# Performance work log

Hardware: AMD Instinct MI355X
Metric: run time of the kernel (lower is better)

Reference implementation:

```python
import jax, jax.numpy as jnp
import numpy as np

B, N, E = 16, 2048, 256


def setup_inputs() -> dict:
    key = jax.random.key(0)
    ks = jax.random.split(key, 9)
    locs = jax.random.uniform(ks[0], (B, N, 2), dtype=jnp.float32)
    probe = jax.random.randint(ks[1], (B, N), 0, 2).astype(bool)
    probe = probe.at[:, 0].set(True)  # guarantee >=1 probe per instance
    s = 0.02
    W_node = jax.random.normal(ks[2], (2, E), dtype=jnp.float32) * s
    b_node = jax.random.normal(ks[3], (E,), dtype=jnp.float32) * s
    W_dist = jax.random.normal(ks[4], (1, E), dtype=jnp.float32) * s
    b_dist = jax.random.normal(ks[5], (E,), dtype=jnp.float32) * s
    W_out = jax.random.normal(ks[6], (2 * E, E), dtype=jnp.float32) * s
    b_out = jax.random.normal(ks[7], (E,), dtype=jnp.float32) * s
    return {
        "locs": locs, "probe": probe,
        "W_node": W_node, "b_node": b_node,
        "W_dist": W_dist, "b_dist": b_dist,
        "W_out": W_out, "b_out": b_out,
    }


def _cdist(x):
    # pairwise euclidean distance [B,N,N] with safe sqrt (0-grad at 0)
    sq = jnp.sum(x * x, axis=-1)                       # [B,N]
    d2 = sq[:, :, None] + sq[:, None, :] - 2.0 * jnp.einsum("bnd,bmd->bnm", x, x)
    d2 = jnp.maximum(d2, 0.0)
    pos = d2 > 0.0
    return jnp.where(pos, jnp.sqrt(jnp.where(pos, d2, 1.0)), 0.0)


def reference(locs, probe, W_node, b_node, W_dist, b_dist, W_out, b_out):
    node_emb = locs @ W_node + b_node                  # [B,N,E]
    dist = _cdist(locs)                                # [B,N,N]
    # rows i that are NOT probes are set to +inf, then min over rows (dim=1)
    dist = jnp.where(probe[:, :, None], dist, jnp.inf)
    min_dist = jnp.min(dist, axis=1)                   # [B,N] dist to nearest probe
    dist_emb = min_dist[..., None] @ W_dist + b_dist   # [B,N,E]
    cat = jnp.concatenate([node_emb, dist_emb], axis=-1)
    return cat @ W_out + b_out                         # [B,N,E]
```

## Files before the change

kernel.cpp:

```cpp
#include <hip/hip_runtime.h>
#include <hip/hip_bf16.h>

#define BSZ  16
#define NPTS 2048
#define EDIM 256
#define QB   64
#define FPB  16

__global__ __launch_bounds__(256) void fold_part(
    const float* __restrict__ Wn,
    const float* __restrict__ bn,
    const float* __restrict__ Wd,
    const float* __restrict__ bd,
    const float* __restrict__ Wo,
    float* __restrict__ ws)
{
    const int e   = threadIdx.x;
    const int blk = blockIdx.x;
    float a = 0.f, b = 0.f, c = 0.f, d = 0.f;
#pragma unroll
    for (int kk = 0; kk < EDIM / FPB; ++kk) {
        const int k = blk * (EDIM / FPB) + kk;
        const float wt = Wo[k * EDIM + e];
        const float wb = Wo[(EDIM + k) * EDIM + e];
        a = fmaf(Wn[k],        wt, a);
        b = fmaf(Wn[EDIM + k], wt, b);
        d = fmaf(bn[k],        wt, d);
        c = fmaf(Wd[k],        wb, c);
        d = fmaf(bd[k],        wb, d);
    }
    float* o = ws + blk * 4 * EDIM;
    o[0 * EDIM + e] = a;
    o[1 * EDIM + e] = b;
    o[2 * EDIM + e] = c;
    o[3 * EDIM + e] = d;
}

__global__ __launch_bounds__(256) void mdpp_main(
    const float* __restrict__ locs,
    const int*   __restrict__ probe,
    const float* __restrict__ ws,
    const float* __restrict__ bo,
    float*       __restrict__ out)
{
    __shared__ __align__(16) float2 plist[NPTS + 2];
    __shared__ float  folded_lds[4 * EDIM];
    __shared__ int    pcount;
    __shared__ float  partmin[4][QB];
    __shared__ float  xq[QB], yq[QB], dq[QB];

    const int t   = threadIdx.x;
    const int bid = blockIdx.x;
    const int b   = bid >> 5;
    const int n0  = (bid & 31) * QB;

    if (t == 0) pcount = 0;
    __syncthreads();

    const float2* lb = reinterpret_cast<const float2*>(locs) + (size_t)b * NPTS;

#pragma unroll
    for (int jj = 0; jj < NPTS / 256; ++jj) {
        const int j = jj * 256 + t;
        if (probe[b * NPTS + j] != 0) {
            const int idx = atomicAdd(&pcount, 1);
            plist[idx] = lb[j];
        }
    }
    if (t < QB) {
        const float2 p = lb[n0 + t];
        xq[t] = p.x;
        yq[t] = p.y;
    }
    __syncthreads();

    if (t == 0) plist[pcount] = make_float2(1.0e19f, 1.0e19f);

#pragma unroll
    for (int v = 0; v < 4; ++v) {
        float s = 0.f;
#pragma unroll
        for (int p = 0; p < FPB; ++p) s += ws[p * 4 * EDIM + v * EDIM + t];
        if (v == 3) s += bo[t];
        folded_lds[v * EDIM + t] = s;
    }
    __syncthreads();

    const int M = pcount;
    const int q = t & (QB - 1);
    const int h = t >> 6;
    const float x = xq[q], y = yq[q];

    float best = 3.0e38f;
    const int npair = (M + 1) >> 1;
    const int lo = (npair * h) >> 2;
    const int hi = (npair * (h + 1)) >> 2;
    const float4* pl4 = reinterpret_cast<const float4*>(plist);
#pragma unroll 2
    for (int j = lo; j < hi; ++j) {
        const float4 pp = pl4[j];
        const float dx0 = x - pp.x, dy0 = y - pp.y;
        const float dx1 = x - pp.z, dy1 = y - pp.w;
        best = fminf(best, fmaf(dy0, dy0, dx0 * dx0));
        best = fminf(best, fmaf(dy1, dy1, dx1 * dx1));
    }
    partmin[h][q] = best;
    __syncthreads();

    if (t < QB) {
        const float m = fminf(fminf(partmin[0][t], partmin[1][t]),
                              fminf(partmin[2][t], partmin[3][t]));
        dq[t] = sqrtf(m);
    }
    __syncthreads();

    const int e0 = (t & 31) * 8;
    float A[8], Bv[8], C[8], D[8];
#pragma unroll
    for (int i = 0; i < 8; ++i) {
        A[i]  = folded_lds[0 * EDIM + e0 + i];
        Bv[i] = folded_lds[1 * EDIM + e0 + i];
        C[i]  = folded_lds[2 * EDIM + e0 + i];
        D[i]  = folded_lds[3 * EDIM + e0 + i];
    }
    const int qh = t >> 5;
#pragma unroll
    for (int it = 0; it < 8; ++it) {
        const int qq = it * 8 + qh;
        const float xx = xq[qq], yy = yq[qq], dd = dq[qq];
        float4 st0, st1;
        st0.x = fmaf(xx, A[0], fmaf(yy, Bv[0], fmaf(dd, C[0], D[0])));
        st0.y = fmaf(xx, A[1], fmaf(yy, Bv[1], fmaf(dd, C[1], D[1])));
        st0.z = fmaf(xx, A[2], fmaf(yy, Bv[2], fmaf(dd, C[2], D[2])));
        st0.w = fmaf(xx, A[3], fmaf(yy, Bv[3], fmaf(dd, C[3], D[3])));
        st1.x = fmaf(xx, A[4], fmaf(yy, Bv[4], fmaf(dd, C[4], D[4])));
        st1.y = fmaf(xx, A[5], fmaf(yy, Bv[5], fmaf(dd, C[5], D[5])));
        st1.z = fmaf(xx, A[6], fmaf(yy, Bv[6], fmaf(dd, C[6], D[6])));
        st1.w = fmaf(xx, A[7], fmaf(yy, Bv[7], fmaf(dd, C[7], D[7])));
        float* op = out + ((size_t)(b * NPTS + n0 + qq) * EDIM + e0);
        *reinterpret_cast<float4*>(op)     = st0;
        *reinterpret_cast<float4*>(op + 4) = st1;
    }
}

extern "C" void kernel_launch(void* const* d_in, const int* in_sizes, int n_in,
                              void* d_out, int out_size, void* d_ws, size_t ws_size,
                              hipStream_t stream) {
    const float* locs  = (const float*)d_in[0];
    const int*   probe = (const int*)d_in[1];
    const float* Wn = (const float*)d_in[2];
    const float* bn = (const float*)d_in[3];
    const float* Wd = (const float*)d_in[4];
    const float* bd = (const float*)d_in[5];
    const float* Wo = (const float*)d_in[6];
    const float* bo = (const float*)d_in[7];
    float* out = (float*)d_out;

    float* partials = (float*)d_ws;

    fold_part<<<FPB, 256, 0, stream>>>(Wn, bn, Wd, bd, Wo, partials);
    mdpp_main<<<BSZ * (NPTS / QB), 256, 0, stream>>>(locs, probe, partials, bo, out);
}
```

Before: 95.73 us.

## Compact probe list once per batch and register-block the nearest-probe search

```diff
diff --git a/kernel.cpp b/kernel.cpp
--- a/kernel.cpp
+++ b/kernel.cpp
@@ -1,5 +1,4 @@
 #include <hip/hip_runtime.h>
-#include <hip/hip_bf16.h>
 
 #define BSZ  16
 #define NPTS 2048
@@ -7,139 +6,164 @@
 #define QB   64
 #define FPB  16
 
-__global__ __launch_bounds__(256) void fold_part(
+
+__global__ __launch_bounds__(256) void prep(
     const float* __restrict__ Wn,
     const float* __restrict__ bn,
     const float* __restrict__ Wd,
     const float* __restrict__ bd,
     const float* __restrict__ Wo,
-    float* __restrict__ ws)
+    const float* __restrict__ locs,
+    const int*   __restrict__ probe,
+    float*  __restrict__ partials,
+    int*    __restrict__ gcnt,
+    float2* __restrict__ glist)
 {
-    const int e   = threadIdx.x;
+    __shared__ int cnt;
+    const int t   = threadIdx.x;
     const int blk = blockIdx.x;
-    float a = 0.f, b = 0.f, c = 0.f, d = 0.f;
+
+    if (blk < FPB) {
+        const int e = t;
+        float a = 0.f, b = 0.f, c = 0.f, d = 0.f;
 #pragma unroll
-    for (int kk = 0; kk < EDIM / FPB; ++kk) {
-        const int k = blk * (EDIM / FPB) + kk;
-        const float wt = Wo[k * EDIM + e];
-        const float wb = Wo[(EDIM + k) * EDIM + e];
-        a = fmaf(Wn[k],        wt, a);
-        b = fmaf(Wn[EDIM + k], wt, b);
-        d = fmaf(bn[k],        wt, d);
-        c = fmaf(Wd[k],        wb, c);
-        d = fmaf(bd[k],        wb, d);
+        for (int kk = 0; kk < EDIM / FPB; ++kk) {
+            const int k = blk * (EDIM / FPB) + kk;
+            const float wt = Wo[k * EDIM + e];
+            const float wb = Wo[(EDIM + k) * EDIM + e];
+            a = fmaf(Wn[k],        wt, a);
+            b = fmaf(Wn[EDIM + k], wt, b);
+            d = fmaf(bn[k],        wt, d);
+            c = fmaf(Wd[k],        wb, c);
+            d = fmaf(bd[k],        wb, d);
+        }
+        float* o = partials + blk * 4 * EDIM;
+        o[0 * EDIM + e] = a;
+        o[1 * EDIM + e] = b;
+        o[2 * EDIM + e] = c;
+        o[3 * EDIM + e] = d;
+    } else {
+        const int b = blk - FPB;
+        if (t == 0) cnt = 0;
+        __syncthreads();
+        const float2* lb = reinterpret_cast<const float2*>(locs) + (size_t)b * NPTS;
+        float2* gl = glist + (size_t)b * NPTS;
+        const int lane = t & 63;
+#pragma unroll
+        for (int jj = 0; jj < NPTS / 256; ++jj) {
+            const int j = jj * 256 + t;
+            const float2 p = lb[j];
+            const bool pred = probe[b * NPTS + j] != 0;
+            const unsigned long long mb = __ballot(pred);
+            const int rank = __popcll(mb & ((1ull << lane) - 1ull));
+            int base = 0;
+            if (lane == 0) base = atomicAdd(&cnt, __popcll(mb));
+            base = __shfl(base, 0);
+            if (pred) gl[base + rank] = p;
+        }
+        __syncthreads();
+        if (t == 0) gcnt[b] = cnt;
     }
-    float* o = ws + blk * 4 * EDIM;
-    o[0 * EDIM + e] = a;
-    o[1 * EDIM + e] = b;
-    o[2 * EDIM + e] = c;
-    o[3 * EDIM + e] = d;
 }
 
 __global__ __launch_bounds__(256) void mdpp_main(
-    const float* __restrict__ locs,
-    const int*   __restrict__ probe,
-    const float* __restrict__ ws,
-    const float* __restrict__ bo,
-    float*       __restrict__ out)
+    const float*  __restrict__ locs,
+    const float*  __restrict__ partials,
+    const int*    __restrict__ gcnt,
+    const float2* __restrict__ glist,
+    const float*  __restrict__ bo,
+    float*        __restrict__ out)
 {
-    __shared__ __align__(16) float2 plist[NPTS + 2];
-    __shared__ float  folded_lds[4 * EDIM];
-    __shared__ int    pcount;
-    __shared__ float  partmin[4][QB];
-    __shared__ float  xq[QB], yq[QB], dq[QB];
+    __shared__ __align__(16) float2 pl[NPTS + 32];
+    __shared__ float folded[4 * EDIM];
+    __shared__ float partmin[16][QB];
+    __shared__ float xq[QB], yq[QB], dq[QB];
 
-    const int t   = threadIdx.x;
-    const int bid = blockIdx.x;
-    const int b   = bid >> 5;
-    const int n0  = (bid & 31) * QB;
+    const int t    = threadIdx.x;
+    const int bid  = blockIdx.x;
+    const int b    = bid >> 5;
+    const int n0   = (bid & 31) * QB;
+    const int lane = t & 63;
+    const int w    = t >> 6;
 
-    if (t == 0) pcount = 0;
-    __syncthreads();
+    const int M  = gcnt[b];
+    const int Mp = (M + 31) & ~31;
 
-    const float2* lb = reinterpret_cast<const float2*>(locs) + (size_t)b * NPTS;
+    const float2* gl = glist + (size_t)b * NPTS;
+    for (int i = t; i < M; i += 256) pl[i] = gl[i];
+    if (t < Mp - M) pl[M + t] = make_float2(1.0e19f, 1.0e19f);
 
 #pragma unroll
-    for (int jj = 0; jj < NPTS / 256; ++jj) {
-        const int j = jj * 256 + t;
-        if (probe[b * NPTS + j] != 0) {
-            const int idx = atomicAdd(&pcount, 1);
-            plist[idx] = lb[j];
-        }
+    for (int v = 0; v < 4; ++v) {
+        float s = 0.f;
+#pragma unroll
+        for (int p = 0; p < FPB; ++p) s += partials[p * 4 * EDIM + v * EDIM + t];
+        if (v == 3) s += bo[t];
+        folded[v * EDIM + t] = s;
     }
+
     if (t < QB) {
-        const float2 p = lb[n0 + t];
+        const float2 p = reinterpret_cast<const float2*>(locs)[(size_t)b * NPTS + n0 + t];
         xq[t] = p.x;
         yq[t] = p.y;
     }
     __syncthreads();
 
-    if (t == 0) plist[pcount] = make_float2(1.0e19f, 1.0e19f);
-
+    const int qb    = lane & 15;
+    const int chunk = w * 4 + (lane >> 4);
+    float qx[4], qy[4], best[4];
 #pragma unroll
-    for (int v = 0; v < 4; ++v) {
-        float s = 0.f;
+    for (int j = 0; j < 4; ++j) {
+        qx[j] = xq[j * 16 + qb];
+        qy[j] = yq[j * 16 + qb];
+        best[j] = 3.0e38f;
+    }
+    const int S2 = Mp >> 5;
+    const float4* pl4 = reinterpret_cast<const float4*>(pl);
+    const int lo = chunk * S2, hi = lo + S2;
+#pragma unroll 2
+    for (int i = lo; i < hi; ++i) {
+        const float4 pp = pl4[i];
 #pragma unroll
-        for (int p = 0; p < FPB; ++p) s += ws[p * 4 * EDIM + v * EDIM + t];
-        if (v == 3) s += bo[t];
-        folded_lds[v * EDIM + t] = s;
+        for (int j = 0; j < 4; ++j) {
+            const float dx0 = qx[j] - pp.x, dy0 = qy[j] - pp.y;
+            const float dx1 = qx[j] - pp.z, dy1 = qy[j] - pp.w;
+            best[j] = fminf(best[j], fmaf(dy0, dy0, dx0 * dx0));
+            best[j] = fminf(best[j], fmaf(dy1, dy1, dx1 * dx1));
+        }
     }
-    __syncthreads();
-
-    const int M = pcount;
-    const int q = t & (QB - 1);
-    const int h = t >> 6;
-    const float x = xq[q], y = yq[q];
-
-    float best = 3.0e38f;
-    const int npair = (M + 1) >> 1;
-    const int lo = (npair * h) >> 2;
-    const int hi = (npair * (h + 1)) >> 2;
-    const float4* pl4 = reinterpret_cast<const float4*>(plist);
-#pragma unroll 2
-    for (int j = lo; j < hi; ++j) {
-        const float4 pp = pl4[j];
-        const float dx0 = x - pp.x, dy0 = y - pp.y;
-        const float dx1 = x - pp.z, dy1 = y - pp.w;
-        best = fminf(best, fmaf(dy0, dy0, dx0 * dx0));
-        best = fminf(best, fmaf(dy1, dy1, dx1 * dx1));
-    }
-    partmin[h][q] = best;
+#pragma unroll
+    for (int j = 0; j < 4; ++j) partmin[chunk][j * 16 + qb] = best[j];
     __syncthreads();
 
     if (t < QB) {
-        const float m = fminf(fminf(partmin[0][t], partmin[1][t]),
-                              fminf(partmin[2][t], partmin[3][t]));
+        float m = partmin[0][t];
+#pragma unroll
+        for (int c = 1; c < 16; ++c) m = fminf(m, partmin[c][t]);
         dq[t] = sqrtf(m);
     }
     __syncthreads();
 
-    const int e0 = (t & 31) * 8;
-    float A[8], Bv[8], C[8], D[8];
+    const int e0 = lane * 4;
+    float A[4], Bv[4], C[4], D[4];
 #pragma unroll
-    for (int i = 0; i < 8; ++i) {
-        A[i]  = folded_lds[0 * EDIM + e0 + i];
-        Bv[i] = folded_lds[1 * EDIM + e0 + i];
-        C[i]  = folded_lds[2 * EDIM + e0 + i];
-        D[i]  = folded_lds[3 * EDIM + e0 + i];
+    for (int i = 0; i < 4; ++i) {
+        A[i]  = folded[0 * EDIM + e0 + i];
+        Bv[i] = folded[1 * EDIM + e0 + i];
+        C[i]  = folded[2 * EDIM + e0 + i];
+        D[i]  = folded[3 * EDIM + e0 + i];
     }
-    const int qh = t >> 5;
 #pragma unroll
-    for (int it = 0; it < 8; ++it) {
-        const int qq = it * 8 + qh;
-        const float xx = xq[qq], yy = yq[qq], dd = dq[qq];
-        float4 st0, st1;
-        st0.x = fmaf(xx, A[0], fmaf(yy, Bv[0], fmaf(dd, C[0], D[0])));
-        st0.y = fmaf(xx, A[1], fmaf(yy, Bv[1], fmaf(dd, C[1], D[1])));
-        st0.z = fmaf(xx, A[2], fmaf(yy, Bv[2], fmaf(dd, C[2], D[2])));
-        st0.w = fmaf(xx, A[3], fmaf(yy, Bv[3], fmaf(dd, C[3], D[3])));
-        st1.x = fmaf(xx, A[4], fmaf(yy, Bv[4], fmaf(dd, C[4], D[4])));
-        st1.y = fmaf(xx, A[5], fmaf(yy, Bv[5], fmaf(dd, C[5], D[5])));
-        st1.z = fmaf(xx, A[6], fmaf(yy, Bv[6], fmaf(dd, C[6], D[6])));
-        st1.w = fmaf(xx, A[7], fmaf(yy, Bv[7], fmaf(dd, C[7], D[7])));
-        float* op = out + ((size_t)(b * NPTS + n0 + qq) * EDIM + e0);
-        *reinterpret_cast<float4*>(op)     = st0;
-        *reinterpret_cast<float4*>(op + 4) = st1;
+    for (int it = 0; it < 16; ++it) {
+        const int r = it * 4 + w;
+        const float xx = xq[r], yy = yq[r], dd = dq[r];
+        float4 st;
+        st.x = fmaf(xx, A[0], fmaf(yy, Bv[0], fmaf(dd, C[0], D[0])));
+        st.y = fmaf(xx, A[1], fmaf(yy, Bv[1], fmaf(dd, C[1], D[1])));
+        st.z = fmaf(xx, A[2], fmaf(yy, Bv[2], fmaf(dd, C[2], D[2])));
+        st.w = fmaf(xx, A[3], fmaf(yy, Bv[3], fmaf(dd, C[3], D[3])));
+        *reinterpret_cast<float4*>(
+            out + ((size_t)(b * NPTS + n0 + r) * EDIM + e0)) = st;
     }
 }
 
@@ -156,8 +180,12 @@
     const float* bo = (const float*)d_in[7];
     float* out = (float*)d_out;
 
-    float* partials = (float*)d_ws;
+    float*  partials = (float*)d_ws;
+    int*    gcnt     = (int*)((char*)d_ws + 65536);
+    float2* glist    = (float2*)((char*)d_ws + 65792);
 
-    fold_part<<<FPB, 256, 0, stream>>>(Wn, bn, Wd, bd, Wo, partials);
-    mdpp_main<<<BSZ * (NPTS / QB), 256, 0, stream>>>(locs, probe, partials, bo, out);
+    prep<<<2 * FPB, 256, 0, stream>>>(Wn, bn, Wd, bd, Wo, locs, probe,
+                                      partials, gcnt, glist);
+    mdpp_main<<<BSZ * (NPTS / QB), 256, 0, stream>>>(locs, partials, gcnt,
+                                                     glist, bo, out);
 }
```

Measured after the change: 90.90 us. -5.0%, faster.
